# Optimization experiments

Hardware: AMD Instinct MI355X
Metric: run time of the kernel (lower is better)

The kernel has to match this reference:

```python
import jax, jax.numpy as jnp
import numpy as np
from math import sqrt

B, N, D = 16, 4096, 128
M = 64 * 24  # mem_size_per_joint * num_joints


def setup_inputs() -> dict:
    key = jax.random.key(0)
    kx, km = jax.random.split(key)
    x = jax.random.normal(kx, (B, N, D), dtype=jnp.float32)
    mem = jax.random.normal(km, (1, D, M), dtype=jnp.float32)  # N(0,1) init as in torch
    return {"x": x, "mem": mem}


def reference(x, mem):
    # x: (B, N, D); mem: (1, D, M)
    d = x.shape[-1]
    w = mem[0]  # (D, M)
    # logits = bmm(m_key (B,M,D), x_ (B,D,N)) / sqrt(D)  -> (B, M, N)
    logits = jnp.einsum('dm,bnd->bmn', w, x) / sqrt(d)
    # softmax over the memory axis (dim=1 in torch layout)
    attn = jax.nn.softmax(logits, axis=1)  # (B, M, N)
    # x_new = bmm(m (B,D,M), attn) -> (B,D,N); output permuted to (B,N,D)
    out = jnp.einsum('dm,bmn->bnd', w, attn)
    return out
```

## Files before the change

kernel.cpp:

```cpp
#include <hip/hip_runtime.h>
#include <math.h>


#define Bdim 16
#define Ndim 4096
#define Ddim 128
#define Mdim 1536
#define NT 64
#define NTHREADS 256
#define NSESS 24
#define SESS_M 64
#define XPAD 136
#define PPAD 72
#define NFRAG 24576

typedef __attribute__((ext_vector_type(8))) _Float16 f16x8;
typedef __attribute__((ext_vector_type(4))) _Float16 f16x4;
typedef __attribute__((ext_vector_type(4))) float    f32x4;

__global__ void jamb_prep(const float* __restrict__ w,
                          _Float16* __restrict__ wt,
                          _Float16* __restrict__ wd) {
    const int tid = blockIdx.x * 256 + threadIdx.x;
    const float SC = 0.12751742957f;
    if (tid < NFRAG) {
        const int f    = tid;
        const int lane = f & 63;
        const int fs   = f >> 6;
        const int ks   = fs & 3;
        const int mt   = fs >> 2;
        const int m    = mt * 16 + (lane & 15);
        const int d0   = ks * 32 + (lane >> 4) * 8;
        f16x8 pk;
        #pragma unroll
        for (int j = 0; j < 8; ++j)
            pk[j] = (_Float16)(w[(size_t)(d0 + j) * Mdim + m] * SC);
        *(f16x8*)&wt[(size_t)f * 8] = pk;
    } else {
        const int f    = tid - NFRAG;
        const int lane = f & 63;
        const int fs   = f >> 6;
        const int km   = fs % 48;
        const int dt   = fs / 48;
        const int d    = dt * 16 + (lane & 15);
        const int m0   = km * 32 + (lane >> 4) * 8;
        const float* src = w + (size_t)d * Mdim + m0;
        const float4 v0 = *(const float4*)src;
        const float4 v1 = *(const float4*)(src + 4);
        f16x8 pk;
        pk[0] = (_Float16)v0.x; pk[1] = (_Float16)v0.y;
        pk[2] = (_Float16)v0.z; pk[3] = (_Float16)v0.w;
        pk[4] = (_Float16)v1.x; pk[5] = (_Float16)v1.y;
        pk[6] = (_Float16)v1.z; pk[7] = (_Float16)v1.w;
        *(f16x8*)&wd[(size_t)f * 8] = pk;
    }
}

__global__ __launch_bounds__(NTHREADS, 4)
void jamb_mfma_kernel(const float* __restrict__ x,
                      const _Float16* __restrict__ wt,
                      const _Float16* __restrict__ wd,
                      float* __restrict__ out) {
    __shared__ __align__(16) _Float16 xs[NT * XPAD];
    __shared__ __align__(16) _Float16 Pbuf[2][NT * PPAD];
    __shared__ float redsum[4][4][16];

    const int t    = threadIdx.x;
    const int w    = t >> 6;
    const int l    = t & 63;
    const int c16  = l & 15;
    const int quad = l >> 4;

    const int blk   = blockIdx.x;
    const int b     = blk >> 6;
    const int nbase = (blk & 63) * NT;

    {
        const float* xb = x + (size_t)(b * Ndim + nbase) * Ddim;
        #pragma unroll
        for (int i = 0; i < 8; ++i) {
            const int f   = t + i * 256;
            const int row = f >> 5;
            const int c4  = (f & 31) * 4;
            const float4 v = *(const float4*)(xb + row * Ddim + c4);
            f16x4 pk;
            pk[0] = (_Float16)v.x; pk[1] = (_Float16)v.y;
            pk[2] = (_Float16)v.z; pk[3] = (_Float16)v.w;
            *(f16x4*)&xs[row * XPAD + c4] = pk;
        }
    }
    __syncthreads();

    const f16x8* WT = (const f16x8*)wt;
    const f16x8* WD = (const f16x8*)wd;

    float sums[4] = {0.f, 0.f, 0.f, 0.f};
    f32x4 c[2][4];
    #pragma unroll
    for (int i = 0; i < 2; ++i)
        #pragma unroll
        for (int nt = 0; nt < 4; ++nt) c[i][nt] = (f32x4){0.f, 0.f, 0.f, 0.f};

    f16x8 fh[4];

    auto p1load = [&](int sess) {
        const int mt = sess * 4 + w;
        #pragma unroll
        for (int s = 0; s < 4; ++s)
            fh[s] = WT[(mt * 4 + s) * 64 + l];
    };

    auto p1 = [&](int sess) {
        f32x4 acc[4];
        #pragma unroll
        for (int nt = 0; nt < 4; ++nt) acc[nt] = (f32x4){0.f, 0.f, 0.f, 0.f};
        #pragma unroll
        for (int s = 0; s < 4; ++s) {
            f16x8 bx[4];
            #pragma unroll
            for (int nt = 0; nt < 4; ++nt)
                bx[nt] = *(const f16x8*)&xs[(nt * 16 + c16) * XPAD + s * 32 + quad * 8];
            #pragma unroll
            for (int nt = 0; nt < 4; ++nt)
                acc[nt] = __builtin_amdgcn_mfma_f32_16x16x32_f16(fh[s], bx[nt], acc[nt], 0, 0, 0);
        }
        _Float16* Pw = &Pbuf[sess & 1][0];
        const int mloc = w * 16 + quad * 4;
        #pragma unroll
        for (int nt = 0; nt < 4; ++nt) {
            const float e0 = exp2f(acc[nt][0]);
            const float e1 = exp2f(acc[nt][1]);
            const float e2 = exp2f(acc[nt][2]);
            const float e3 = exp2f(acc[nt][3]);
            sums[nt] += (e0 + e1) + (e2 + e3);
            f16x4 pk;
            pk[0] = (_Float16)e0; pk[1] = (_Float16)e1;
            pk[2] = (_Float16)e2; pk[3] = (_Float16)e3;
            *(f16x4*)&Pw[(nt * 16 + c16) * PPAD + mloc] = pk;
        }
    };

    auto p2 = [&](int q) {
        const _Float16* Pr = &Pbuf[q & 1][0];
        #pragma unroll
        for (int sk = 0; sk < 2; ++sk) {
            const f16x8 a0 = WD[((2 * w)     * 48 + q * 2 + sk) * 64 + l];
            const f16x8 a1 = WD[((2 * w + 1) * 48 + q * 2 + sk) * 64 + l];
            f16x8 p[4];
            #pragma unroll
            for (int nt = 0; nt < 4; ++nt)
                p[nt] = *(const f16x8*)&Pr[(nt * 16 + c16) * PPAD + sk * 32 + quad * 8];
            #pragma unroll
            for (int nt = 0; nt < 4; ++nt) {
                c[0][nt] = __builtin_amdgcn_mfma_f32_16x16x32_f16(a0, p[nt], c[0][nt], 0, 0, 0);
                c[1][nt] = __builtin_amdgcn_mfma_f32_16x16x32_f16(a1, p[nt], c[1][nt], 0, 0, 0);
            }
        }
    };

    p1load(0);
    p1(0);
    #pragma unroll 1
    for (int q = 0; q < NSESS - 1; ++q) {
        __syncthreads();
        p1load(q + 1);
        p2(q);
        p1(q + 1);
    }
    __syncthreads();
    p2(NSESS - 1);

    #pragma unroll
    for (int nt = 0; nt < 4; ++nt) {
        sums[nt] += __shfl_xor(sums[nt], 16, 64);
        sums[nt] += __shfl_xor(sums[nt], 32, 64);
    }
    if (quad == 0) {
        #pragma unroll
        for (int nt = 0; nt < 4; ++nt) redsum[w][nt][c16] = sums[nt];
    }
    __syncthreads();

    float inv[4];
    #pragma unroll
    for (int nt = 0; nt < 4; ++nt)
        inv[nt] = 1.f / ((redsum[0][nt][c16] + redsum[1][nt][c16]) +
                         (redsum[2][nt][c16] + redsum[3][nt][c16]));

    #pragma unroll
    for (int dt2 = 0; dt2 < 2; ++dt2) {
        #pragma unroll
        for (int nt = 0; nt < 4; ++nt) {
            float* op = out + (size_t)(b * Ndim + nbase + nt * 16 + c16) * Ddim
                           + (2 * w + dt2) * 16 + quad * 4;
            float4 o;
            o.x = c[dt2][nt][0] * inv[nt];
            o.y = c[dt2][nt][1] * inv[nt];
            o.z = c[dt2][nt][2] * inv[nt];
            o.w = c[dt2][nt][3] * inv[nt];
            *(float4*)op = o;
        }
    }
}

extern "C" void kernel_launch(void* const* d_in, const int* in_sizes, int n_in,
                              void* d_out, int out_size, void* d_ws, size_t ws_size,
                              hipStream_t stream) {
    const float* x = (const float*)d_in[0];
    const float* w = (const float*)d_in[1];
    float* out = (float*)d_out;
    (void)in_sizes; (void)n_in; (void)out_size; (void)ws_size;

    _Float16* wt = (_Float16*)d_ws;
    _Float16* wd = wt + Ddim * Mdim;

    jamb_prep<<<dim3((2 * NFRAG) / 256), dim3(256), 0, stream>>>(w, wt, wd);
    jamb_mfma_kernel<<<dim3((Bdim * Ndim) / NT), dim3(NTHREADS), 0, stream>>>(x, wt, wd, out);
}
```

Before: 144.0 us.

## Switch to 32x32x16 MFMA tiles with x fragments held in registers

```diff
diff --git a/kernel.cpp b/kernel.cpp
--- a/kernel.cpp
+++ b/kernel.cpp
@@ -9,14 +9,12 @@
 #define NT 64
 #define NTHREADS 256
 #define NSESS 24
-#define SESS_M 64
-#define XPAD 136
-#define PPAD 72
+#define PPAD 68
 #define NFRAG 24576
 
-typedef __attribute__((ext_vector_type(8))) _Float16 f16x8;
-typedef __attribute__((ext_vector_type(4))) _Float16 f16x4;
-typedef __attribute__((ext_vector_type(4))) float    f32x4;
+typedef __attribute__((ext_vector_type(8)))  _Float16 f16x8;
+typedef __attribute__((ext_vector_type(4)))  _Float16 f16x4;
+typedef __attribute__((ext_vector_type(16))) float    f32x16;
 
 __global__ void jamb_prep(const float* __restrict__ w,
                           _Float16* __restrict__ wt,
@@ -25,12 +23,12 @@
     const float SC = 0.12751742957f;
     if (tid < NFRAG) {
         const int f    = tid;
-        const int lane = f & 63;
+        const int l    = f & 63;
         const int fs   = f >> 6;
-        const int ks   = fs & 3;
-        const int mt   = fs >> 2;
-        const int m    = mt * 16 + (lane & 15);
-        const int d0   = ks * 32 + (lane >> 4) * 8;
+        const int ks   = fs & 7;
+        const int mt   = fs >> 3;
+        const int m    = mt * 32 + (l & 31);
+        const int d0   = ks * 16 + (l >> 5) * 8;
         f16x8 pk;
         #pragma unroll
         for (int j = 0; j < 8; ++j)
@@ -38,12 +36,12 @@
         *(f16x8*)&wt[(size_t)f * 8] = pk;
     } else {
         const int f    = tid - NFRAG;
-        const int lane = f & 63;
+        const int l    = f & 63;
         const int fs   = f >> 6;
-        const int km   = fs % 48;
-        const int dt   = fs / 48;
-        const int d    = dt * 16 + (lane & 15);
-        const int m0   = km * 32 + (lane >> 4) * 8;
+        const int km   = fs % 96;
+        const int dt   = fs / 96;
+        const int d    = dt * 32 + (l & 31);
+        const int m0   = km * 16 + (l >> 5) * 8;
         const float* src = w + (size_t)d * Mdim + m0;
         const float4 v0 = *(const float4*)src;
         const float4 v1 = *(const float4*)(src + 4);
@@ -61,143 +59,115 @@
                       const _Float16* __restrict__ wt,
                       const _Float16* __restrict__ wd,
                       float* __restrict__ out) {
-    __shared__ __align__(16) _Float16 xs[NT * XPAD];
     __shared__ __align__(16) _Float16 Pbuf[2][NT * PPAD];
-    __shared__ float redsum[4][4][16];
+    __shared__ float redsum[2][2][32];
 
     const int t    = threadIdx.x;
     const int w    = t >> 6;
     const int l    = t & 63;
-    const int c16  = l & 15;
-    const int quad = l >> 4;
+    const int l31  = l & 31;
+    const int hi   = l >> 5;
+    const int w1   = w & 1;
+    const int wm   = w >> 1;
 
     const int blk   = blockIdx.x;
     const int b     = blk >> 6;
     const int nbase = (blk & 63) * NT;
 
+    f16x8 bx[8];
     {
-        const float* xb = x + (size_t)(b * Ndim + nbase) * Ddim;
+        const float* xb = x + (size_t)(b * Ndim + nbase + w1 * 32 + l31) * Ddim;
         #pragma unroll
-        for (int i = 0; i < 8; ++i) {
-            const int f   = t + i * 256;
-            const int row = f >> 5;
-            const int c4  = (f & 31) * 4;
-            const float4 v = *(const float4*)(xb + row * Ddim + c4);
-            f16x4 pk;
-            pk[0] = (_Float16)v.x; pk[1] = (_Float16)v.y;
-            pk[2] = (_Float16)v.z; pk[3] = (_Float16)v.w;
-            *(f16x4*)&xs[row * XPAD + c4] = pk;
+        for (int ks = 0; ks < 8; ++ks) {
+            const float* s = xb + ks * 16 + hi * 8;
+            const float4 v0 = *(const float4*)s;
+            const float4 v1 = *(const float4*)(s + 4);
+            f16x8 pk;
+            pk[0] = (_Float16)v0.x; pk[1] = (_Float16)v0.y;
+            pk[2] = (_Float16)v0.z; pk[3] = (_Float16)v0.w;
+            pk[4] = (_Float16)v1.x; pk[5] = (_Float16)v1.y;
+            pk[6] = (_Float16)v1.z; pk[7] = (_Float16)v1.w;
+            bx[ks] = pk;
         }
     }
-    __syncthreads();
 
     const f16x8* WT = (const f16x8*)wt;
     const f16x8* WD = (const f16x8*)wd;
 
-    float sums[4] = {0.f, 0.f, 0.f, 0.f};
-    f32x4 c[2][4];
-    #pragma unroll
-    for (int i = 0; i < 2; ++i)
+    float ssum = 0.f;
+    f32x16 c0 = (f32x16)(0.f);
+    f32x16 c1 = (f32x16)(0.f);
+    const int prow = (w1 * 32 + l31) * PPAD;
+
+    auto p1 = [&](int q) {
+        f32x16 acc = (f32x16)(0.f);
         #pragma unroll
-        for (int nt = 0; nt < 4; ++nt) c[i][nt] = (f32x4){0.f, 0.f, 0.f, 0.f};
-
-    f16x8 fh[4];
-
-    auto p1load = [&](int sess) {
-        const int mt = sess * 4 + w;
+        for (int ks = 0; ks < 8; ++ks) {
+            const f16x8 fh = WT[(size_t)((2 * q + wm) * 8 + ks) * 64 + l];
+            acc = __builtin_amdgcn_mfma_f32_32x32x16_f16(fh, bx[ks], acc, 0, 0, 0);
+        }
+        _Float16* Pw = &Pbuf[q & 1][0];
         #pragma unroll
-        for (int s = 0; s < 4; ++s)
-            fh[s] = WT[(mt * 4 + s) * 64 + l];
-    };
-
-    auto p1 = [&](int sess) {
-        f32x4 acc[4];
-        #pragma unroll
-        for (int nt = 0; nt < 4; ++nt) acc[nt] = (f32x4){0.f, 0.f, 0.f, 0.f};
-        #pragma unroll
-        for (int s = 0; s < 4; ++s) {
-            f16x8 bx[4];
-            #pragma unroll
-            for (int nt = 0; nt < 4; ++nt)
-                bx[nt] = *(const f16x8*)&xs[(nt * 16 + c16) * XPAD + s * 32 + quad * 8];
-            #pragma unroll
-            for (int nt = 0; nt < 4; ++nt)
-                acc[nt] = __builtin_amdgcn_mfma_f32_16x16x32_f16(fh[s], bx[nt], acc[nt], 0, 0, 0);
-        }
-        _Float16* Pw = &Pbuf[sess & 1][0];
-        const int mloc = w * 16 + quad * 4;
-        #pragma unroll
-        for (int nt = 0; nt < 4; ++nt) {
-            const float e0 = exp2f(acc[nt][0]);
-            const float e1 = exp2f(acc[nt][1]);
-            const float e2 = exp2f(acc[nt][2]);
-            const float e3 = exp2f(acc[nt][3]);
-            sums[nt] += (e0 + e1) + (e2 + e3);
+        for (int g = 0; g < 4; ++g) {
+            const float e0 = exp2f(acc[g * 4 + 0]);
+            const float e1 = exp2f(acc[g * 4 + 1]);
+            const float e2 = exp2f(acc[g * 4 + 2]);
+            const float e3 = exp2f(acc[g * 4 + 3]);
+            ssum += (e0 + e1) + (e2 + e3);
             f16x4 pk;
             pk[0] = (_Float16)e0; pk[1] = (_Float16)e1;
             pk[2] = (_Float16)e2; pk[3] = (_Float16)e3;
-            *(f16x4*)&Pw[(nt * 16 + c16) * PPAD + mloc] = pk;
+            *(f16x4*)&Pw[prow + wm * 32 + g * 8 + hi * 4] = pk;
         }
     };
 
     auto p2 = [&](int q) {
         const _Float16* Pr = &Pbuf[q & 1][0];
         #pragma unroll
-        for (int sk = 0; sk < 2; ++sk) {
-            const f16x8 a0 = WD[((2 * w)     * 48 + q * 2 + sk) * 64 + l];
-            const f16x8 a1 = WD[((2 * w + 1) * 48 + q * 2 + sk) * 64 + l];
-            f16x8 p[4];
-            #pragma unroll
-            for (int nt = 0; nt < 4; ++nt)
-                p[nt] = *(const f16x8*)&Pr[(nt * 16 + c16) * PPAD + sk * 32 + quad * 8];
-            #pragma unroll
-            for (int nt = 0; nt < 4; ++nt) {
-                c[0][nt] = __builtin_amdgcn_mfma_f32_16x16x32_f16(a0, p[nt], c[0][nt], 0, 0, 0);
-                c[1][nt] = __builtin_amdgcn_mfma_f32_16x16x32_f16(a1, p[nt], c[1][nt], 0, 0, 0);
-            }
+        for (int sk = 0; sk < 4; ++sk) {
+            const f16x8 a = WD[(size_t)(w * 96 + q * 4 + sk) * 64 + l];
+            const f16x4 p0lo = *(const f16x4*)&Pr[l31 * PPAD + sk * 16 + hi * 8];
+            const f16x4 p0hi = *(const f16x4*)&Pr[l31 * PPAD + sk * 16 + hi * 8 + 4];
+            const f16x4 p1lo = *(const f16x4*)&Pr[(32 + l31) * PPAD + sk * 16 + hi * 8];
+            const f16x4 p1hi = *(const f16x4*)&Pr[(32 + l31) * PPAD + sk * 16 + hi * 8 + 4];
+            const f16x8 pf0 = __builtin_shufflevector(p0lo, p0hi, 0, 1, 2, 3, 4, 5, 6, 7);
+            const f16x8 pf1 = __builtin_shufflevector(p1lo, p1hi, 0, 1, 2, 3, 4, 5, 6, 7);
+            c0 = __builtin_amdgcn_mfma_f32_32x32x16_f16(a, pf0, c0, 0, 0, 0);
+            c1 = __builtin_amdgcn_mfma_f32_32x32x16_f16(a, pf1, c1, 0, 0, 0);
         }
     };
 
-    p1load(0);
     p1(0);
     #pragma unroll 1
     for (int q = 0; q < NSESS - 1; ++q) {
         __syncthreads();
-        p1load(q + 1);
         p2(q);
         p1(q + 1);
     }
     __syncthreads();
     p2(NSESS - 1);
 
+    ssum += __shfl_xor(ssum, 32, 64);
+    if (hi == 0) redsum[w1][wm][l31] = ssum;
+    __syncthreads();
+    float inv[2];
     #pragma unroll
-    for (int nt = 0; nt < 4; ++nt) {
-        sums[nt] += __shfl_xor(sums[nt], 16, 64);
-        sums[nt] += __shfl_xor(sums[nt], 32, 64);
-    }
-    if (quad == 0) {
-        #pragma unroll
-        for (int nt = 0; nt < 4; ++nt) redsum[w][nt][c16] = sums[nt];
-    }
-    __syncthreads();
-
-    float inv[4];
-    #pragma unroll
-    for (int nt = 0; nt < 4; ++nt)
-        inv[nt] = 1.f / ((redsum[0][nt][c16] + redsum[1][nt][c16]) +
-                         (redsum[2][nt][c16] + redsum[3][nt][c16]));
+    for (int tt = 0; tt < 2; ++tt)
+        inv[tt] = 1.f / (redsum[tt][0][l31] + redsum[tt][1][l31]);
 
     #pragma unroll
-    for (int dt2 = 0; dt2 < 2; ++dt2) {
+    for (int tt = 0; tt < 2; ++tt) {
+        const float iv = inv[tt];
+        const f32x16 cc = tt ? c1 : c0;
         #pragma unroll
-        for (int nt = 0; nt < 4; ++nt) {
-            float* op = out + (size_t)(b * Ndim + nbase + nt * 16 + c16) * Ddim
-                           + (2 * w + dt2) * 16 + quad * 4;
+        for (int g = 0; g < 4; ++g) {
+            float* op = out + (size_t)(b * Ndim + nbase + tt * 32 + l31) * Ddim
+                            + w * 32 + g * 8 + hi * 4;
             float4 o;
-            o.x = c[dt2][nt][0] * inv[nt];
-            o.y = c[dt2][nt][1] * inv[nt];
-            o.z = c[dt2][nt][2] * inv[nt];
-            o.w = c[dt2][nt][3] * inv[nt];
+            o.x = cc[g * 4 + 0] * iv;
+            o.y = cc[g * 4 + 1] * iv;
+            o.z = cc[g * 4 + 2] * iv;
+            o.w = cc[g * 4 + 3] * iv;
             *(float4*)op = o;
         }
     }
```

Result: slower. 171.8 us (+19.3%).
